# Optimization experiments

Measured on AMD Instinct MI355X. Metric: run time of the kernel, lower is better.

Reference implementation:

```python
import jax, jax.numpy as jnp
import numpy as np

N = 65536      # nodes
E = 1048576    # edges (avg degree 16)
L = 24         # input_length == lstm input size == lstm num_layers
H = 64         # lstm hidden


def _lin_init(key, fi, fo):
    return jax.random.normal(key, (fi, fo), jnp.float32) / np.sqrt(fi)


def setup_inputs() -> dict:
    key = jax.random.key(0)
    ks = iter(jax.random.split(key, 64))
    d = {}
    d["x"] = jax.random.normal(next(ks), (N, 421 + L), jnp.float32)
    d["edge_index"] = jax.random.randint(next(ks), (2, E), 0, N)

    def lin(fi, fo):
        return _lin_init(next(ks), fi, fo), jnp.zeros((fo,), jnp.float32)

    d["poi1_W"], d["poi1_b"] = lin(13, 64)
    d["poi2_W"], d["poi2_b"] = lin(64, 64)
    d["svi1_W"], d["svi1_b"] = lin(365, 128)
    d["svi2_W"], d["svi2_b"] = lin(128, 128)
    d["all1_W"], d["all1_b"] = lin(192, 128)
    d["all2_W"], d["all2_b"] = lin(128, 128)
    for name, fi, fo in (("gat1", 128, 128), ("gat2", 128, 128), ("gat3", 128, 64)):
        d[name + "_W"], d[name + "_b"] = lin(fi, fo)
        d[name + "_asrc"] = jax.random.normal(next(ks), (fo,), jnp.float32) / np.sqrt(fo)
        d[name + "_adst"] = jax.random.normal(next(ks), (fo,), jnp.float32) / np.sqrt(fo)
    d["lstm_Wih0"] = jax.random.normal(next(ks), (L, 4 * H), jnp.float32) / np.sqrt(L)
    d["lstm_Wih"] = jax.random.normal(next(ks), (L - 1, H, 4 * H), jnp.float32) / np.sqrt(H)
    d["lstm_Whh"] = jax.random.normal(next(ks), (L, H, 4 * H), jnp.float32) / np.sqrt(H)
    d["lstm_b"] = jnp.zeros((L, 4 * H), jnp.float32)
    d["time1_W"], d["time1_b"] = lin(64, 64)
    d["time2_W"], d["time2_b"] = lin(64, 64)
    d["lin1_W"], d["lin1_b"] = lin(128, 64)
    d["lin2_W"], d["lin2_b"] = lin(64, 64)
    d["lin3_W"], d["lin3_b"] = lin(64, 1)
    return d


def _gat(h_in, W, a_src, a_dst, b, src, dst, n):
    # PyG GATConv (1 head): gather -> per-edge attn -> segment softmax -> scatter
    h = h_in @ W                                   # [N, F]
    s = h @ a_src                                  # [N]
    t = h @ a_dst                                  # [N]
    e = jax.nn.leaky_relu(s[src] + t[dst], 0.2)    # [E']
    m = jax.ops.segment_max(e, dst, num_segments=n)
    ee = jnp.exp(e - m[dst])
    denom = jax.ops.segment_sum(ee, dst, num_segments=n)
    alpha = ee / denom[dst]
    out = jax.ops.segment_sum(h[src] * alpha[:, None], dst, num_segments=n)
    return out + b


def _forward(x, poi1_W, poi1_b, poi2_W, poi2_b, svi1_W, svi1_b, svi2_W, svi2_b,
             all1_W, all1_b, all2_W, all2_b,
             gat1_W, gat1_b, gat1_asrc, gat1_adst,
             gat2_W, gat2_b, gat2_asrc, gat2_adst,
             gat3_W, gat3_b, gat3_asrc, gat3_adst,
             lstm_Wih0, lstm_Wih, lstm_Whh, lstm_b,
             time1_W, time1_b, time2_W, time2_b,
             lin1_W, lin1_b, lin2_W, lin2_b, lin3_W, lin3_b,
             edge_index):
    n = x.shape[0]
    relu = jax.nn.relu
    # feature-branch MLPs
    x_poi = relu(relu(x[:, 3:16] @ poi1_W + poi1_b) @ poi2_W + poi2_b)
    x_svi = relu(relu(x[:, 56:421] @ svi1_W + svi1_b) @ svi2_W + svi2_b)
    h = jnp.concatenate([x_poi, x_svi], axis=1)
    h = relu(relu(h @ all1_W + all1_b) @ all2_W + all2_b)
    # add self loops once (PyG GATConv default add_self_loops=True)
    loops = jnp.arange(n, dtype=edge_index.dtype)
    src = jnp.concatenate([edge_index[0], loops])
    dst = jnp.concatenate([edge_index[1], loops])
    h = relu(_gat(h, gat1_W, gat1_asrc, gat1_adst, gat1_b, src, dst, n))
    h = relu(_gat(h, gat2_W, gat2_asrc, gat2_adst, gat2_b, src, dst, n))
    h = relu(_gat(h, gat3_W, gat3_asrc, gat3_adst, gat3_b, src, dst, n))
    # stacked LSTM over the single timestep t (h0=c0=0 -> f gate & Whh contribute 0)
    inp = x[:, 421:]                               # [N, L]
    hs = []
    for l in range(L):
        Wih = lstm_Wih0 if l == 0 else lstm_Wih[l - 1]
        gates = inp @ Wih + lstm_b[l]              # [N, 4H], torch gate order i,f,g,o
        i, f, g, o = jnp.split(gates, 4, axis=-1)
        c = jax.nn.sigmoid(i) * jnp.tanh(g)
        h_l = jax.nn.sigmoid(o) * jnp.tanh(c)
        hs.append(h_l)
        inp = h_l
    t = hs[2]                                      # hn[2]
    t = relu(relu(t @ time1_W + time1_b) @ time2_W + time2_b)
    z = jnp.concatenate([h, t], axis=1)            # [N, 128]
    z = relu(z @ lin1_W + lin1_b)
    z = relu(z @ lin2_W + lin2_b)
    return z @ lin3_W + lin3_b                     # [N, 1]


def reference(x, edge_index, poi1_W, poi1_b, poi2_W, poi2_b, svi1_W, svi1_b,
              svi2_W, svi2_b, all1_W, all1_b, all2_W, all2_b,
              gat1_W, gat1_b, gat1_asrc, gat1_adst,
              gat2_W, gat2_b, gat2_asrc, gat2_adst,
              gat3_W, gat3_b, gat3_asrc, gat3_adst,
              lstm_Wih0, lstm_Wih, lstm_Whh, lstm_b,
              time1_W, time1_b, time2_W, time2_b,
              lin1_W, lin1_b, lin2_W, lin2_b, lin3_W, lin3_b):
    return _forward(x, poi1_W, poi1_b, poi2_W, poi2_b, svi1_W, svi1_b, svi2_W, svi2_b,
                    all1_W, all1_b, all2_W, all2_b,
                    gat1_W, gat1_b, gat1_asrc, gat1_adst,
                    gat2_W, gat2_b, gat2_asrc, gat2_adst,
                    gat3_W, gat3_b, gat3_asrc, gat3_adst,
                    lstm_Wih0, lstm_Wih, lstm_Whh, lstm_b,
                    time1_W, time1_b, time2_W, time2_b,
                    lin1_W, lin1_b, lin2_W, lin2_b, lin3_W, lin3_b,
                    edge_index)
```

## Files before the change

kernel.cpp:

```cpp
#include <hip/hip_runtime.h>
#include <math.h>

#define DEV __device__ __forceinline__

typedef __attribute__((ext_vector_type(8))) short short8;
typedef __attribute__((ext_vector_type(4))) float f32x4;
typedef float f32x4u __attribute__((ext_vector_type(4), aligned(4)));
typedef __attribute__((ext_vector_type(4))) unsigned int u32x4;
typedef __attribute__((ext_vector_type(4))) _Float16 h16x4;

#define NEG_BIG (-3.0e38f)
#define CAPB 4096
#define CHUNK 4096

DEV float sigm(float x) { return 1.0f / (1.0f + __expf(-x)); }
DEV float leaky(float e) { return (e >= 0.0f) ? e : 0.2f * e; }

DEV void split_bf16(const float f[8], short8& hi, short8& lo) {
#pragma unroll
  for (int i = 0; i < 8; ++i) {
    unsigned u = __builtin_bit_cast(unsigned, f[i]);
    hi[i] = (short)(u >> 16);
    float h = __builtin_bit_cast(float, u & 0xffff0000u);
    float r = f[i] - h;
    lo[i] = (short)(__builtin_bit_cast(unsigned, r) >> 16);
  }
}

DEV unsigned packsplit(float v) {
  unsigned u = __builtin_bit_cast(unsigned, v);
  unsigned hf = u & 0xffff0000u;
  float r = v - __builtin_bit_cast(float, hf);
  return hf | (__builtin_bit_cast(unsigned, r) >> 16);
}

DEV void unpack_pk(const u32x4 p0, const u32x4 p1, short8& hi, short8& lo) {
  u32x4 h, l;
  h[0] = __builtin_amdgcn_perm(p0[1], p0[0], 0x07060302u);
  h[1] = __builtin_amdgcn_perm(p0[3], p0[2], 0x07060302u);
  h[2] = __builtin_amdgcn_perm(p1[1], p1[0], 0x07060302u);
  h[3] = __builtin_amdgcn_perm(p1[3], p1[2], 0x07060302u);
  l[0] = __builtin_amdgcn_perm(p0[1], p0[0], 0x05040100u);
  l[1] = __builtin_amdgcn_perm(p0[3], p0[2], 0x05040100u);
  l[2] = __builtin_amdgcn_perm(p1[1], p1[0], 0x05040100u);
  l[3] = __builtin_amdgcn_perm(p1[3], p1[2], 0x05040100u);
  hi = __builtin_bit_cast(short8, h);
  lo = __builtin_bit_cast(short8, l);
}

template <int G, int MT, int NT>
DEV void mfma_grp(f32x4 (&acc)[MT][NT], const short8 (&ah)[MT],
                  const short8 (&al)[MT], const short8 (&bh)[4],
                  const short8 (&bl)[4]) {
#pragma unroll
  for (int mt = 0; mt < MT; ++mt)
#pragma unroll
    for (int j = 0; j < 4; ++j) {
      acc[mt][G * 4 + j] = __builtin_amdgcn_mfma_f32_16x16x32_bf16(
          ah[mt], bh[j], acc[mt][G * 4 + j], 0, 0, 0);
      acc[mt][G * 4 + j] = __builtin_amdgcn_mfma_f32_16x16x32_bf16(
          ah[mt], bl[j], acc[mt][G * 4 + j], 0, 0, 0);
      acc[mt][G * 4 + j] = __builtin_amdgcn_mfma_f32_16x16x32_bf16(
          al[mt], bh[j], acc[mt][G * 4 + j], 0, 0, 0);
    }
}


__global__ void fill_i32_kernel(int* p, int v, int n) {
  int i = blockIdx.x * blockDim.x + threadIdx.x;
  if (i < n) p[i] = v;
}


__global__ __launch_bounds__(256) void bucket_bin(
    const int* __restrict__ ei, int* __restrict__ bucket_cnt,
    unsigned* __restrict__ ebuf, int E, int Et) {
  __shared__ unsigned stage[CHUNK];
  __shared__ int hist[512], rbase[512], lcur[512];
  const int tid = threadIdx.x;
  const long long e0 = (long long)blockIdx.x * CHUNK;
  const int nalive = (int)((Et - e0) < CHUNK ? (Et - e0) : CHUNK);
  for (int i = tid; i < 512; i += 256) hist[i] = 0;
  __syncthreads();
  for (int k = tid; k < nalive; k += 256) {
    long long e = e0 + k;
    int s, d;
    if (e < E) { s = ei[e]; d = ei[E + e]; } else { s = (int)(e - E); d = s; }
    unsigned p = (unsigned)s | ((unsigned)d << 16);
    stage[k] = p;
    atomicAdd(&hist[d >> 7], 1);
  }
  __syncthreads();
  for (int i = tid; i < 512; i += 256) {
    int c = hist[i];
    rbase[i] = c ? atomicAdd(&bucket_cnt[i], c) : 0;
    lcur[i] = 0;
  }
  __syncthreads();
  for (int k = tid; k < nalive; k += 256) {
    unsigned p = stage[k];
    int b = (int)(p >> 23);
    int lofs = atomicAdd(&lcur[b], 1);
    int pos = rbase[b] + lofs;
    if (pos < CAPB) ebuf[(long long)b * CAPB + pos] = p;
  }
}

__global__ __launch_bounds__(512) void bucket_scan(
    const int* __restrict__ cnt, int* __restrict__ start, int Et) {
  __shared__ int sh[512];
  int tid = threadIdx.x;
  int v = cnt[tid];
  sh[tid] = v;
  __syncthreads();
  int val = v;
  for (int off = 1; off < 512; off <<= 1) {
    int add = (tid >= off) ? sh[tid - off] : 0;
    __syncthreads();
    val += add;
    sh[tid] = val;
    __syncthreads();
  }
  start[tid] = val - v;
  if (tid == 511) start[512] = Et;
}

__global__ __launch_bounds__(128) void bucket_csr(
    const unsigned* __restrict__ ebuf, const int* __restrict__ bucket_cnt,
    const int* __restrict__ bucket_start, int* __restrict__ row_start,
    int* __restrict__ srcs, int N, int Et) {
  __shared__ unsigned stage[CAPB];
  __shared__ int hist[128], hbase[128], lcur[128];
  const int b = blockIdx.x, tid = threadIdx.x;
  int cnt = bucket_cnt[b];
  cnt = cnt < CAPB ? cnt : CAPB;
  const int gbase = bucket_start[b];
  hist[tid] = 0;
  __syncthreads();
  const unsigned* eb = ebuf + (long long)b * CAPB;
  for (int k = tid; k < cnt; k += 128) {
    unsigned p = eb[k];
    stage[k] = p;
    atomicAdd(&hist[(p >> 16) & 127], 1);
  }
  __syncthreads();
  int v = hist[tid];
  hbase[tid] = v;
  __syncthreads();
  int val = v;
  for (int off = 1; off < 128; off <<= 1) {
    int add = (tid >= off) ? hbase[tid - off] : 0;
    __syncthreads();
    val += add;
    hbase[tid] = val;
    __syncthreads();
  }
  int ex = val - v;
  row_start[b * 128 + tid] = gbase + ex;
  __syncthreads();
  hbase[tid] = ex;
  lcur[tid] = 0;
  __syncthreads();
  for (int k = tid; k < cnt; k += 128) {
    unsigned p = stage[k];
    int o = (p >> 16) & 127;
    int lofs = atomicAdd(&lcur[o], 1);
    srcs[gbase + hbase[o] + lofs] = (int)(p & 0xffffu);
  }
  if (b == 0 && tid == 0) row_start[N] = Et;
}

struct WJobs {
  const float* W[16];
  short* hi[16];
  short* lo[16];
  int K[16];
  int M16[16];
  int ldw[16];
  int skip[16];
  int tile0[16];
};

__global__ __launch_bounds__(64) void wsplit_all(WJobs jb, int njobs) {
  int b = blockIdx.x;
  int ji = 0;
#pragma unroll
  for (int i = 1; i < 16; ++i)
    if (i < njobs && b >= jb.tile0[i]) ji = i;
  int t = b - jb.tile0[ji];
  int M16 = jb.M16[ji];
  int kc = t / M16, ntG = t % M16;
  int K = jb.K[ji], ldw = jb.ldw[ji];
  const float* __restrict__ W = jb.W[ji];

  int lane = threadIdx.x;
  int kb = kc * 32 + (lane >> 4) * 8;
  int c = ntG * 16 + (lane & 15);
  if (jb.skip[ji] && c >= 64) c += 64;
  float f[8];
#pragma unroll
  for (int j = 0; j < 8; ++j) {
    int k = kb + j;
    f[j] = (k < K) ? W[(long long)k * ldw + c] : 0.0f;
  }
  short8 h, l;
  split_bf16(f, h, l);
  long long off = ((long long)t * 64 + lane) * 8;
  *(short8*)(jb.hi[ji] + off) = h;
  *(short8*)(jb.lo[ji] + off) = l;
}

template <int MT, int NT, int APK, int OPK, int STE>
__global__ __launch_bounds__(64) void gemm_mfma(
    const void* __restrict__ Av, int lda,
    const short* __restrict__ wh, const short* __restrict__ wl,
    const float* __restrict__ bias,
    void* __restrict__ Cv, int ldc,
    int K, int KC, int act,
    const float* __restrict__ asrc, const float* __restrict__ adst,
    float* __restrict__ sOut, float* __restrict__ tOut) {
  const int lane = threadIdx.x;
  const int m = lane & 15, q = lane >> 4;
  const long long r0 = (long long)blockIdx.x * (MT * 16);

  f32x4 acc[MT][NT];
#pragma unroll
  for (int i = 0; i < MT; ++i)
#pragma unroll
    for (int j = 0; j < NT; ++j) acc[i][j] = (f32x4)(0.0f);

  u32x4 pA[MT][2];
  float fA[MT][8];

  auto loadA = [&](int kc) {
#pragma unroll
    for (int mt = 0; mt < MT; ++mt) {
      if (APK == 1) {
        const unsigned* ap =
            (const unsigned*)Av + (r0 + mt * 16 + m) * lda + kc * 32 + q * 8;
        pA[mt][0] = *(const u32x4*)ap;
        pA[mt][1] = *(const u32x4*)(ap + 4);
      } else {
        const float* ap =
            (const float*)Av + (r0 + mt * 16 + m) * lda + kc * 32 + q * 8;
        if (kc * 32 + 32 <= K) {
          f32x4u p0 = *(const f32x4u*)ap;
          f32x4u p1 = *(const f32x4u*)(ap + 4);
#pragma unroll
          for (int j = 0; j < 4; ++j) { fA[mt][j] = p0[j]; fA[mt][4 + j] = p1[j]; }
        } else {
#pragma unroll
          for (int j = 0; j < 8; ++j) {
            int k = kc * 32 + q * 8 + j;
            fA[mt][j] = (k < K) ? ap[j] : 0.0f;
          }
        }
      }
    }
  };

  short8 ah[MT], al[MT];
  auto unpackA = [&]() {
#pragma unroll
    for (int mt = 0; mt < MT; ++mt) {
      if (APK == 1)
        unpack_pk(pA[mt][0], pA[mt][1], ah[mt], al[mt]);
      else
        split_bf16(fA[mt], ah[mt], al[mt]);
    }
  };

  short8 bh0[4], bl0[4], bh1[4], bl1[4];
  auto loadB = [&](short8 (&bh)[4], short8 (&bl)[4], int kc, int g) {
#pragma unroll
    for (int j = 0; j < 4; ++j) {
      long long off = (((long long)kc * NT + (g * 4 + j)) * 64 + lane) * 8;
      bh[j] = *(const short8*)(wh + off);
      bl[j] = *(const short8*)(wl + off);
    }
  };

  if constexpr (NT == 4) {
    loadA(0);
    loadB(bh0, bl0, 0, 0);
    int kc = 0;
    for (; kc + 2 <= KC; kc += 2) {
      unpackA();
      loadB(bh1, bl1, kc + 1, 0);
      loadA(kc + 1);
      mfma_grp<0, MT, NT>(acc, ah, al, bh0, bl0);
      unpackA();
      if (kc + 2 < KC) {
        loadB(bh0, bl0, kc + 2, 0);
        loadA(kc + 2);
      }
      mfma_grp<0, MT, NT>(acc, ah, al, bh1, bl1);
    }
    if (kc < KC) {
      unpackA();
      mfma_grp<0, MT, NT>(acc, ah, al, bh0, bl0);
    }
  } else {
    loadA(0);
    loadB(bh0, bl0, 0, 0);
    for (int kc = 0; kc < KC; ++kc) {
      unpackA();
      loadB(bh1, bl1, kc, 1);
      if (kc + 1 < KC) loadA(kc + 1);
      mfma_grp<0, MT, NT>(acc, ah, al, bh0, bl0);
      if (kc + 1 < KC) loadB(bh0, bl0, kc + 1, 0);
      mfma_grp<1, MT, NT>(acc, ah, al, bh1, bl1);
    }
  }

  if (STE == 2) {
    float w3[NT], bs[NT];
#pragma unroll
    for (int nt = 0; nt < NT; ++nt) {
      int col = nt * 16 + m;
      w3[nt] = asrc[col];
      bs[nt] = bias[col];
    }
#pragma unroll
    for (int mt = 0; mt < MT; ++mt)
#pragma unroll
      for (int reg = 0; reg < 4; ++reg) {
        float ps = 0.0f;
#pragma unroll
        for (int nt = 0; nt < NT; ++nt) {
          float v = fmaxf(acc[mt][nt][reg] + bs[nt], 0.0f);
          ps = fmaf(v, w3[nt], ps);
        }
#pragma unroll
        for (int off = 1; off < 16; off <<= 1) ps += __shfl_xor(ps, off, 64);
        if (m == 0) sOut[r0 + mt * 16 + q * 4 + reg] = ps + adst[0];
      }
    return;
  }

#pragma unroll
  for (int nt = 0; nt < NT; ++nt) {
    int col = nt * 16 + m;
    float bsv = bias ? bias[col] : 0.0f;
#pragma unroll
    for (int mt = 0; mt < MT; ++mt) {
      long long rb = r0 + mt * 16 + q * 4;
#pragma unroll
      for (int reg = 0; reg < 4; ++reg) {
        float v = acc[mt][nt][reg] + bsv;
        if (act == 1) v = fmaxf(v, 0.0f);
        if (OPK == 1)
          ((unsigned*)Cv)[(rb + reg) * ldc + col] = packsplit(v);
        else if (OPK == 2)
          ((_Float16*)Cv)[(rb + reg) * ldc + col] = (_Float16)v;
        else
          ((float*)Cv)[(rb + reg) * ldc + col] = v;
      }
    }
  }

  if (STE == 1) {
    float as[NT], ad[NT];
#pragma unroll
    for (int nt = 0; nt < NT; ++nt) {
      int col = nt * 16 + m;
      as[nt] = asrc[col];
      ad[nt] = adst[col];
    }
#pragma unroll
    for (int mt = 0; mt < MT; ++mt)
#pragma unroll
      for (int reg = 0; reg < 4; ++reg) {
        float ps = 0.0f, pt = 0.0f;
#pragma unroll
        for (int nt = 0; nt < NT; ++nt) {
          ps = fmaf(acc[mt][nt][reg], as[nt], ps);
          pt = fmaf(acc[mt][nt][reg], ad[nt], pt);
        }
#pragma unroll
        for (int off = 1; off < 16; off <<= 1) {
          ps += __shfl_xor(ps, off, 64);
          pt += __shfl_xor(pt, off, 64);
        }
        if (m == 0) {
          long long r = r0 + mt * 16 + q * 4 + reg;
          sOut[r] = ps;
          tOut[r] = pt;
        }
      }
  }
}

template <int APK>
__global__ __launch_bounds__(64) void gemm_lstm(
    const void* __restrict__ Av, int lda,
    const short* __restrict__ wh, const short* __restrict__ wl,
    const float* __restrict__ bias,
    unsigned* __restrict__ H,
    int K, int KC) {
  const int lane = threadIdx.x;
  const int m = lane & 15, q = lane >> 4;
  const long long r0 = (long long)blockIdx.x * 16;

  f32x4 acc[12];
#pragma unroll
  for (int j = 0; j < 12; ++j) acc[j] = (f32x4)(0.0f);

  u32x4 pA[2];
  float fA[8];

  auto loadA = [&](int kc) {
    if (APK == 1) {
      const unsigned* ap = (const unsigned*)Av + (r0 + m) * lda + kc * 32 + q * 8;
      pA[0] = *(const u32x4*)ap;
      pA[1] = *(const u32x4*)(ap + 4);
    } else {
      const float* ap = (const float*)Av + (r0 + m) * lda + kc * 32 + q * 8;
      if (kc * 32 + 32 <= K) {
        f32x4u p0 = *(const f32x4u*)ap;
        f32x4u p1 = *(const f32x4u*)(ap + 4);
#pragma unroll
        for (int j = 0; j < 4; ++j) { fA[j] = p0[j]; fA[4 + j] = p1[j]; }
      } else {
#pragma unroll
        for (int j = 0; j < 8; ++j) {
          int k = kc * 32 + q * 8 + j;
          fA[j] = (k < K) ? ap[j] : 0.0f;
        }
      }
    }
  };

  short8 bh0, bl0, bh1, bl1;
  auto loadB = [&](short8& bh, short8& bl, int kc, int nt) {
    long long off = (((long long)kc * 12 + nt) * 64 + lane) * 8;
    bh = *(const short8*)(wh + off);
    bl = *(const short8*)(wl + off);
  };

  loadA(0);
  loadB(bh0, bl0, 0, 0);
  for (int kc = 0; kc < KC; ++kc) {
    short8 ah, al;
    if (APK == 1)
      unpack_pk(pA[0], pA[1], ah, al);
    else
      split_bf16(fA, ah, al);
    loadB(bh1, bl1, kc, 1);
    if (kc + 1 < KC) loadA(kc + 1);
    const int kn = (kc + 1 < KC) ? kc + 1 : kc;
#pragma unroll
    for (int nt = 0; nt < 12; ++nt) {
      short8& cbh = (nt & 1) ? bh1 : bh0;
      short8& cbl = (nt & 1) ? bl1 : bl0;
      acc[nt] = __builtin_amdgcn_mfma_f32_16x16x32_bf16(ah, cbh, acc[nt], 0, 0, 0);
      acc[nt] = __builtin_amdgcn_mfma_f32_16x16x32_bf16(ah, cbl, acc[nt], 0, 0, 0);
      acc[nt] = __builtin_amdgcn_mfma_f32_16x16x32_bf16(al, cbh, acc[nt], 0, 0, 0);
      if (nt + 2 < 12)
        loadB((nt & 1) ? bh1 : bh0, (nt & 1) ? bl1 : bl0, kc, nt + 2);
      else if (nt + 2 == 12)
        loadB(bh0, bl0, kn, 0);
    }
  }

#pragma unroll
  for (int nt = 0; nt < 4; ++nt) {
    int col = nt * 16 + m;
    float bi = bias[col], bg = bias[128 + col], bo = bias[192 + col];
#pragma unroll
    for (int reg = 0; reg < 4; ++reg) {
      float gi = acc[nt][reg] + bi;
      float gg = acc[nt + 4][reg] + bg;
      float go = acc[nt + 8][reg] + bo;
      float cc = sigm(gi) * tanhf(gg);
      H[(r0 + q * 4 + reg) * 64 + col] = packsplit(sigm(go) * tanhf(cc));
    }
  }
}


template <int FO, int OPK>
__global__ __launch_bounds__(256) void gat_agg(
    const _Float16* __restrict__ G, const float* __restrict__ s,
    const float* __restrict__ t, const int* __restrict__ row_start,
    const int* __restrict__ srcs, const float* __restrict__ bias,
    void* __restrict__ outv, int ldc) {
  constexpr int CAP = 128;
  constexpr int LPE = FO / 4;
  constexpr int EPW = 64 / LPE;
  __shared__ float ecache[4][CAP];
  __shared__ int icache[4][CAP];
  const int wv = threadIdx.x >> 6;
  const int lane = threadIdx.x & 63;
  const int d = blockIdx.x * 4 + wv;
  const int start = row_start[d], end = row_start[d + 1];
  const float td = t[d];

  float m = NEG_BIG, dsum = 0.0f;
  for (int j = start + lane; j < end; j += 64) {
    int sj = srcs[j];
    float e = leaky(s[sj] + td);
    int idx = j - start;
    if (idx < CAP) { ecache[wv][idx] = e; icache[wv][idx] = sj; }
    float mn = fmaxf(m, e);
    dsum = dsum * __expf(m - mn) + __expf(e - mn);
    m = mn;
  }
#pragma unroll
  for (int off = 32; off; off >>= 1) {
    float mo = __shfl_xor(m, off, 64);
    float dso = __shfl_xor(dsum, off, 64);
    float mn = fmaxf(m, mo);
    dsum = dsum * __expf(m - mn) + dso * __expf(mo - mn);
    m = mn;
  }
  const float inv = 1.0f / dsum;

  const int deg = end - start;
  const int capdeg = deg < CAP ? deg : CAP;
  for (int idx = lane; idx < capdeg; idx += 64)
    ecache[wv][idx] = __expf(ecache[wv][idx] - m) * inv;
  __syncthreads();

  const int grp = lane / LPE, cl = lane % LPE;
  const _Float16* __restrict__ Gc = G + cl * 4;
  float a0 = 0.0f, a1 = 0.0f, a2 = 0.0f, a3 = 0.0f;
  int idx = grp;
  for (; idx + 3 * EPW < capdeg; idx += 4 * EPW) {
    const int i1 = idx + EPW, i2 = idx + 2 * EPW, i3 = idx + 3 * EPW;
    int s0 = icache[wv][idx], s1 = icache[wv][i1];
    int s2 = icache[wv][i2], s3 = icache[wv][i3];
    float l0 = ecache[wv][idx], l1 = ecache[wv][i1];
    float l2 = ecache[wv][i2], l3 = ecache[wv][i3];
    h16x4 g0 = *(const h16x4*)(Gc + (long long)s0 * FO);
    h16x4 g1 = *(const h16x4*)(Gc + (long long)s1 * FO);
    h16x4 g2 = *(const h16x4*)(Gc + (long long)s2 * FO);
    h16x4 g3 = *(const h16x4*)(Gc + (long long)s3 * FO);
    a0 = fmaf(l0, (float)g0[0], a0); a1 = fmaf(l0, (float)g0[1], a1);
    a2 = fmaf(l0, (float)g0[2], a2); a3 = fmaf(l0, (float)g0[3], a3);
    a0 = fmaf(l1, (float)g1[0], a0); a1 = fmaf(l1, (float)g1[1], a1);
    a2 = fmaf(l1, (float)g1[2], a2); a3 = fmaf(l1, (float)g1[3], a3);
    a0 = fmaf(l2, (float)g2[0], a0); a1 = fmaf(l2, (float)g2[1], a1);
    a2 = fmaf(l2, (float)g2[2], a2); a3 = fmaf(l2, (float)g2[3], a3);
    a0 = fmaf(l3, (float)g3[0], a0); a1 = fmaf(l3, (float)g3[1], a1);
    a2 = fmaf(l3, (float)g3[2], a2); a3 = fmaf(l3, (float)g3[3], a3);
  }
  for (; idx + EPW < capdeg; idx += 2 * EPW) {
    const int i1 = idx + EPW;
    int s0 = icache[wv][idx], s1 = icache[wv][i1];
    float l0 = ecache[wv][idx], l1 = ecache[wv][i1];
    h16x4 g0 = *(const h16x4*)(Gc + (long long)s0 * FO);
    h16x4 g1 = *(const h16x4*)(Gc + (long long)s1 * FO);
    a0 = fmaf(l0, (float)g0[0], a0); a1 = fmaf(l0, (float)g0[1], a1);
    a2 = fmaf(l0, (float)g0[2], a2); a3 = fmaf(l0, (float)g0[3], a3);
    a0 = fmaf(l1, (float)g1[0], a0); a1 = fmaf(l1, (float)g1[1], a1);
    a2 = fmaf(l1, (float)g1[2], a2); a3 = fmaf(l1, (float)g1[3], a3);
  }
  for (; idx < capdeg; idx += EPW) {
    int s0 = icache[wv][idx];
    float l0 = ecache[wv][idx];
    h16x4 g0 = *(const h16x4*)(Gc + (long long)s0 * FO);
    a0 = fmaf(l0, (float)g0[0], a0); a1 = fmaf(l0, (float)g0[1], a1);
    a2 = fmaf(l0, (float)g0[2], a2); a3 = fmaf(l0, (float)g0[3], a3);
  }
  for (; idx < deg; idx += EPW) {
    int s0 = srcs[start + idx];
    float l0 = __expf(leaky(s[s0] + td) - m) * inv;
    h16x4 g0 = *(const h16x4*)(Gc + (long long)s0 * FO);
    a0 = fmaf(l0, (float)g0[0], a0); a1 = fmaf(l0, (float)g0[1], a1);
    a2 = fmaf(l0, (float)g0[2], a2); a3 = fmaf(l0, (float)g0[3], a3);
  }
#pragma unroll
  for (int off = 32; off >= LPE; off >>= 1) {
    a0 += __shfl_xor(a0, off, 64);
    a1 += __shfl_xor(a1, off, 64);
    a2 += __shfl_xor(a2, off, 64);
    a3 += __shfl_xor(a3, off, 64);
  }
  if (grp == 0) {
    f32x4u bs = *(const f32x4u*)(bias + cl * 4);
    float v0 = fmaxf(a0 + bs[0], 0.0f);
    float v1 = fmaxf(a1 + bs[1], 0.0f);
    float v2 = fmaxf(a2 + bs[2], 0.0f);
    float v3 = fmaxf(a3 + bs[3], 0.0f);
    if (OPK == 1) {
      u32x4 pv;
      pv[0] = packsplit(v0); pv[1] = packsplit(v1);
      pv[2] = packsplit(v2); pv[3] = packsplit(v3);
      *(u32x4*)((unsigned*)outv + (long long)d * ldc + cl * 4) = pv;
    } else {
      f32x4u v; v[0] = v0; v[1] = v1; v[2] = v2; v[3] = v3;
      *(f32x4u*)((float*)outv + (long long)d * ldc + cl * 4) = v;
    }
  }
}


struct WSplit { const short* hi; const short* lo; };

extern "C" void kernel_launch(void* const* d_in, const int* in_sizes, int n_in,
                              void* d_out, int out_size, void* d_ws, size_t ws_size,
                              hipStream_t stream) {
  const int N = 65536, E = 1048576;
  const int Et = E + N;

  const float* x        = (const float*)d_in[0];
  const int*   ei       = (const int*)d_in[1];
  const float* poi1_W   = (const float*)d_in[2];
  const float* poi1_b   = (const float*)d_in[3];
  const float* poi2_W   = (const float*)d_in[4];
  const float* poi2_b   = (const float*)d_in[5];
  const float* svi1_W   = (const float*)d_in[6];
  const float* svi1_b   = (const float*)d_in[7];
  const float* svi2_W   = (const float*)d_in[8];
  const float* svi2_b   = (const float*)d_in[9];
  const float* all1_W   = (const float*)d_in[10];
  const float* all1_b   = (const float*)d_in[11];
  const float* all2_W   = (const float*)d_in[12];
  const float* all2_b   = (const float*)d_in[13];
  const float* gat1_W   = (const float*)d_in[14];
  const float* gat1_b   = (const float*)d_in[15];
  const float* gat1_as  = (const float*)d_in[16];
  const float* gat1_ad  = (const float*)d_in[17];
  const float* gat2_W   = (const float*)d_in[18];
  const float* gat2_b   = (const float*)d_in[19];
  const float* gat2_as  = (const float*)d_in[20];
  const float* gat2_ad  = (const float*)d_in[21];
  const float* gat3_W   = (const float*)d_in[22];
  const float* gat3_b   = (const float*)d_in[23];
  const float* gat3_as  = (const float*)d_in[24];
  const float* gat3_ad  = (const float*)d_in[25];
  const float* lstm_Wih0= (const float*)d_in[26];
  const float* lstm_Wih = (const float*)d_in[27];
  const float* lstm_b   = (const float*)d_in[29];
  const float* time1_W  = (const float*)d_in[30];
  const float* time1_b  = (const float*)d_in[31];
  const float* time2_W  = (const float*)d_in[32];
  const float* time2_b  = (const float*)d_in[33];
  const float* lin1_W   = (const float*)d_in[34];
  const float* lin1_b   = (const float*)d_in[35];
  const float* lin2_W   = (const float*)d_in[36];
  const float* lin2_b   = (const float*)d_in[37];
  const float* lin3_W   = (const float*)d_in[38];
  const float* lin3_b   = (const float*)d_in[39];
  float* out = (float*)d_out;

  float* wsf   = (float*)d_ws;
  float* R192  = wsf;
  float* RA    = R192 + (size_t)N * 192;
  float* RA2   = RA + (size_t)N * 64;
  float* RB    = RA + (size_t)N * 128;
  float* Rz    = RB + (size_t)N * 256;
  float* sArr  = Rz + (size_t)N * 128;
  float* tArr  = sArr + N;
  int* ints         = (int*)(tArr + N);
  int* row_start    = ints;
  int* srcs         = row_start + (N + 1);
  int* bucket_cnt   = srcs + Et;
  int* bucket_start = bucket_cnt + 512;
  unsigned* ebuf    = (unsigned*)(bucket_start + 513);
  short* pool = (short*)(((uintptr_t)(ebuf + 512 * CAPB) + 15) & ~(uintptr_t)15);

  WJobs jb{};
  int nj = 0, tiles = 0;
  auto split = [&](const float* W, int K, int M, int ldw, int skip) -> WSplit {
    int KC = (K + 31) / 32;
    size_t sz = (size_t)KC * M * 32;
    short* hi = pool; pool += sz;
    short* lo = pool; pool += sz;
    jb.W[nj] = W; jb.hi[nj] = hi; jb.lo[nj] = lo;
    jb.K[nj] = K; jb.M16[nj] = M / 16; jb.ldw[nj] = ldw; jb.skip[nj] = skip;
    jb.tile0[nj] = tiles;
    tiles += KC * (M / 16);
    ++nj;
    return {hi, lo};
  };

  auto gemm = [&](const void* A, int lda, WSplit w, const float* bias,
                  void* C, int ldc, int K, int M, int act, int apk, int opk) {
    int KC = (K + 31) / 32;
    dim3 grid(N / 16), blk(64);
    if (M == 64) {
      if (apk == 0 && opk == 1)
        hipLaunchKernelGGL((gemm_mfma<1, 4, 0, 1, 0>), grid, blk, 0, stream,
                           A, lda, w.hi, w.lo, bias, C, ldc, K, KC, act,
                           nullptr, nullptr, nullptr, nullptr);
      else if (apk == 1 && opk == 1)
        hipLaunchKernelGGL((gemm_mfma<1, 4, 1, 1, 0>), grid, blk, 0, stream,
                           A, lda, w.hi, w.lo, bias, C, ldc, K, KC, act,
                           nullptr, nullptr, nullptr, nullptr);
      else if (apk == 1 && opk == 0)
        hipLaunchKernelGGL((gemm_mfma<1, 4, 1, 0, 0>), grid, blk, 0, stream,
                           A, lda, w.hi, w.lo, bias, C, ldc, K, KC, act,
                           nullptr, nullptr, nullptr, nullptr);
      else
        hipLaunchKernelGGL((gemm_mfma<1, 4, 0, 0, 0>), grid, blk, 0, stream,
                           A, lda, w.hi, w.lo, bias, C, ldc, K, KC, act,
                           nullptr, nullptr, nullptr, nullptr);
    } else {
      if (apk == 0 && opk == 1)
        hipLaunchKernelGGL((gemm_mfma<1, 8, 0, 1, 0>), grid, blk, 0, stream,
                           A, lda, w.hi, w.lo, bias, C, ldc, K, KC, act,
                           nullptr, nullptr, nullptr, nullptr);
      else if (apk == 1 && opk == 1)
        hipLaunchKernelGGL((gemm_mfma<1, 8, 1, 1, 0>), grid, blk, 0, stream,
                           A, lda, w.hi, w.lo, bias, C, ldc, K, KC, act,
                           nullptr, nullptr, nullptr, nullptr);
      else if (apk == 1 && opk == 0)
        hipLaunchKernelGGL((gemm_mfma<1, 8, 1, 0, 0>), grid, blk, 0, stream,
                           A, lda, w.hi, w.lo, bias, C, ldc, K, KC, act,
                           nullptr, nullptr, nullptr, nullptr);
      else
        hipLaunchKernelGGL((gemm_mfma<1, 8, 0, 0, 0>), grid, blk, 0, stream,
                           A, lda, w.hi, w.lo, bias, C, ldc, K, KC, act,
                           nullptr, nullptr, nullptr, nullptr);
    }
  };
  auto gemm_st = [&](const void* A, WSplit w, void* G, int M,
                     const float* as_, const float* ad_) {
    dim3 grid(N / 16), blk(64);
    if (M == 128)
      hipLaunchKernelGGL((gemm_mfma<1, 8, 1, 2, 1>), grid, blk, 0, stream,
                         A, 128, w.hi, w.lo, (const float*)nullptr,
                         G, 128, 128, 4, 0, as_, ad_, sArr, tArr);
    else
      hipLaunchKernelGGL((gemm_mfma<1, 4, 1, 2, 1>), grid, blk, 0, stream,
                         A, 128, w.hi, w.lo, (const float*)nullptr,
                         G, 64, 128, 4, 0, as_, ad_, sArr, tArr);
  };

  WSplit wpoi1 = split(poi1_W, 13, 64, 64, 0);
  WSplit wpoi2 = split(poi2_W, 64, 64, 64, 0);
  WSplit wsvi1 = split(svi1_W, 365, 128, 128, 0);
  WSplit wsvi2 = split(svi2_W, 128, 128, 128, 0);
  WSplit wall1 = split(all1_W, 192, 128, 128, 0);
  WSplit wall2 = split(all2_W, 128, 128, 128, 0);
  WSplit wg1   = split(gat1_W, 128, 128, 128, 0);
  WSplit wg2   = split(gat2_W, 128, 128, 128, 0);
  WSplit wg3   = split(gat3_W, 128, 64, 64, 0);
  WSplit wls0  = split(lstm_Wih0, 24, 192, 256, 1);
  WSplit wls1  = split(lstm_Wih, 64, 192, 256, 1);
  WSplit wls2  = split(lstm_Wih + 64 * 256, 64, 192, 256, 1);
  WSplit wt1   = split(time1_W, 64, 64, 64, 0);
  WSplit wt2   = split(time2_W, 64, 64, 64, 0);
  WSplit wl1   = split(lin1_W, 128, 64, 64, 0);
  WSplit wl2   = split(lin2_W, 64, 64, 64, 0);
  hipLaunchKernelGGL(wsplit_all, dim3(tiles), dim3(64), 0, stream, jb, nj);

  const int TB = 256;

  hipLaunchKernelGGL(fill_i32_kernel, dim3(2), dim3(TB), 0, stream,
                     bucket_cnt, 0, 512);
  hipLaunchKernelGGL(bucket_bin, dim3((Et + CHUNK - 1) / CHUNK), dim3(256),
                     0, stream, ei, bucket_cnt, ebuf, E, Et);
  hipLaunchKernelGGL(bucket_scan, dim3(1), dim3(512), 0, stream,
                     bucket_cnt, bucket_start, Et);
  hipLaunchKernelGGL(bucket_csr, dim3(512), dim3(128), 0, stream,
                     ebuf, bucket_cnt, bucket_start, row_start, srcs, N, Et);

  gemm(x + 3, 445, wpoi1, poi1_b, RA, 64, 13, 64, 1, 0, 1);
  gemm(RA, 64, wpoi2, poi2_b, R192, 192, 64, 64, 1, 1, 1);
  gemm(x + 56, 445, wsvi1, svi1_b, RB, 128, 365, 128, 1, 0, 1);
  gemm(RB, 128, wsvi2, svi2_b, R192 + 64, 192, 128, 128, 1, 1, 1);
  gemm(R192, 192, wall1, all1_b, RA, 128, 192, 128, 1, 1, 1);
  gemm(RA, 128, wall2, all2_b, RB, 128, 128, 128, 1, 1, 1);

  const int aggBlocks = N / 4;
  _Float16* Gh = (_Float16*)RA;

  gemm_st(RB, wg1, Gh, 128, gat1_as, gat1_ad);
  hipLaunchKernelGGL((gat_agg<128, 1>), dim3(aggBlocks), dim3(256), 0, stream,
                     Gh, sArr, tArr, row_start, srcs, gat1_b, RB, 128);
  gemm_st(RB, wg2, Gh, 128, gat2_as, gat2_ad);
  hipLaunchKernelGGL((gat_agg<128, 1>), dim3(aggBlocks), dim3(256), 0, stream,
                     Gh, sArr, tArr, row_start, srcs, gat2_b, RB, 128);
  gemm_st(RB, wg3, Gh, 64, gat3_as, gat3_ad);
  hipLaunchKernelGGL((gat_agg<64, 1>), dim3(aggBlocks), dim3(256), 0, stream,
                     Gh, sArr, tArr, row_start, srcs, gat3_b, Rz, 128);

  hipLaunchKernelGGL((gemm_lstm<0>), dim3(N / 16), dim3(64), 0, stream,
                     x + 421, 445, wls0.hi, wls0.lo, lstm_b,
                     (unsigned*)RA, 24, 1);
  hipLaunchKernelGGL((gemm_lstm<1>), dim3(N / 16), dim3(64), 0, stream,
                     RA, 64, wls1.hi, wls1.lo, lstm_b + 256,
                     (unsigned*)RA2, 64, 2);
  hipLaunchKernelGGL((gemm_lstm<1>), dim3(N / 16), dim3(64), 0, stream,
                     RA2, 64, wls2.hi, wls2.lo, lstm_b + 512,
                     (unsigned*)RA, 64, 2);

  gemm(RA, 64, wt1, time1_b, RA2, 64, 64, 64, 1, 1, 1);
  gemm(RA2, 64, wt2, time2_b, Rz + 64, 128, 64, 64, 1, 1, 1);

  gemm(Rz, 128, wl1, lin1_b, RA, 64, 128, 64, 1, 1, 1);
  hipLaunchKernelGGL((gemm_mfma<1, 4, 1, 0, 2>), dim3(N / 16), dim3(64), 0, stream,
                     RA, 64, wl2.hi, wl2.lo, lin2_b, nullptr, 64, 64, 2, 0,
                     lin3_W, lin3_b, out, nullptr);
}
```

Baseline: 686.2 us.

## Co-schedule independent GEMM and LSTM branches in combined multi-role kernel launches

```diff
diff --git a/kernel.cpp b/kernel.cpp
--- a/kernel.cpp
+++ b/kernel.cpp
@@ -210,18 +210,24 @@
   *(short8*)(jb.lo[ji] + off) = l;
 }
 
+
+struct GemmArgs {
+  const void* A; const short* wh; const short* wl; const float* bias;
+  void* C; const float* asrc; const float* adst; float* sOut; float* tOut;
+  int lda, ldc, K, KC, act;
+};
+
+struct LstmArgs {
+  const void* A; const short* wh; const short* wl; const float* bias;
+  unsigned* H; int lda, K, KC;
+};
+
 template <int MT, int NT, int APK, int OPK, int STE>
-__global__ __launch_bounds__(64) void gemm_mfma(
-    const void* __restrict__ Av, int lda,
-    const short* __restrict__ wh, const short* __restrict__ wl,
-    const float* __restrict__ bias,
-    void* __restrict__ Cv, int ldc,
-    int K, int KC, int act,
-    const float* __restrict__ asrc, const float* __restrict__ adst,
-    float* __restrict__ sOut, float* __restrict__ tOut) {
+DEV void gemm_body(const GemmArgs& g, int bid) {
   const int lane = threadIdx.x;
   const int m = lane & 15, q = lane >> 4;
-  const long long r0 = (long long)blockIdx.x * (MT * 16);
+  const long long r0 = (long long)bid * (MT * 16);
+  const int K = g.K, KC = g.KC, lda = g.lda;
 
   f32x4 acc[MT][NT];
 #pragma unroll
@@ -237,12 +243,12 @@
     for (int mt = 0; mt < MT; ++mt) {
       if (APK == 1) {
         const unsigned* ap =
-            (const unsigned*)Av + (r0 + mt * 16 + m) * lda + kc * 32 + q * 8;
+            (const unsigned*)g.A + (r0 + mt * 16 + m) * lda + kc * 32 + q * 8;
         pA[mt][0] = *(const u32x4*)ap;
         pA[mt][1] = *(const u32x4*)(ap + 4);
       } else {
         const float* ap =
-            (const float*)Av + (r0 + mt * 16 + m) * lda + kc * 32 + q * 8;
+            (const float*)g.A + (r0 + mt * 16 + m) * lda + kc * 32 + q * 8;
         if (kc * 32 + 32 <= K) {
           f32x4u p0 = *(const f32x4u*)ap;
           f32x4u p1 = *(const f32x4u*)(ap + 4);
@@ -271,12 +277,12 @@
   };
 
   short8 bh0[4], bl0[4], bh1[4], bl1[4];
-  auto loadB = [&](short8 (&bh)[4], short8 (&bl)[4], int kc, int g) {
+  auto loadB = [&](short8 (&bh)[4], short8 (&bl)[4], int kc, int gg) {
 #pragma unroll
     for (int j = 0; j < 4; ++j) {
-      long long off = (((long long)kc * NT + (g * 4 + j)) * 64 + lane) * 8;
-      bh[j] = *(const short8*)(wh + off);
-      bl[j] = *(const short8*)(wl + off);
+      long long off = (((long long)kc * NT + (gg * 4 + j)) * 64 + lane) * 8;
+      bh[j] = *(const short8*)(g.wh + off);
+      bl[j] = *(const short8*)(g.wl + off);
     }
   };
 
@@ -318,8 +324,8 @@
 #pragma unroll
     for (int nt = 0; nt < NT; ++nt) {
       int col = nt * 16 + m;
-      w3[nt] = asrc[col];
-      bs[nt] = bias[col];
+      w3[nt] = g.asrc[col];
+      bs[nt] = g.bias[col];
     }
 #pragma unroll
     for (int mt = 0; mt < MT; ++mt)
@@ -333,7 +339,7 @@
         }
 #pragma unroll
         for (int off = 1; off < 16; off <<= 1) ps += __shfl_xor(ps, off, 64);
-        if (m == 0) sOut[r0 + mt * 16 + q * 4 + reg] = ps + adst[0];
+        if (m == 0) g.sOut[r0 + mt * 16 + q * 4 + reg] = ps + g.adst[0];
       }
     return;
   }
@@ -341,20 +347,20 @@
 #pragma unroll
   for (int nt = 0; nt < NT; ++nt) {
     int col = nt * 16 + m;
-    float bsv = bias ? bias[col] : 0.0f;
+    float bsv = g.bias ? g.bias[col] : 0.0f;
 #pragma unroll
     for (int mt = 0; mt < MT; ++mt) {
       long long rb = r0 + mt * 16 + q * 4;
 #pragma unroll
       for (int reg = 0; reg < 4; ++reg) {
         float v = acc[mt][nt][reg] + bsv;
-        if (act == 1) v = fmaxf(v, 0.0f);
+        if (g.act == 1) v = fmaxf(v, 0.0f);
         if (OPK == 1)
-          ((unsigned*)Cv)[(rb + reg) * ldc + col] = packsplit(v);
+          ((unsigned*)g.C)[(rb + reg) * g.ldc + col] = packsplit(v);
         else if (OPK == 2)
-          ((_Float16*)Cv)[(rb + reg) * ldc + col] = (_Float16)v;
+          ((_Float16*)g.C)[(rb + reg) * g.ldc + col] = (_Float16)v;
         else
-          ((float*)Cv)[(rb + reg) * ldc + col] = v;
+          ((float*)g.C)[(rb + reg) * g.ldc + col] = v;
       }
     }
   }
@@ -364,8 +370,8 @@
 #pragma unroll
     for (int nt = 0; nt < NT; ++nt) {
       int col = nt * 16 + m;
-      as[nt] = asrc[col];
-      ad[nt] = adst[col];
+      as[nt] = g.asrc[col];
+      ad[nt] = g.adst[col];
     }
 #pragma unroll
     for (int mt = 0; mt < MT; ++mt)
@@ -384,23 +390,19 @@
         }
         if (m == 0) {
           long long r = r0 + mt * 16 + q * 4 + reg;
-          sOut[r] = ps;
-          tOut[r] = pt;
+          g.sOut[r] = ps;
+          g.tOut[r] = pt;
         }
       }
   }
 }
 
 template <int APK>
-__global__ __launch_bounds__(64) void gemm_lstm(
-    const void* __restrict__ Av, int lda,
-    const short* __restrict__ wh, const short* __restrict__ wl,
-    const float* __restrict__ bias,
-    unsigned* __restrict__ H,
-    int K, int KC) {
+DEV void lstm_body(const LstmArgs& g, int bid) {
   const int lane = threadIdx.x;
   const int m = lane & 15, q = lane >> 4;
-  const long long r0 = (long long)blockIdx.x * 16;
+  const long long r0 = (long long)bid * 16;
+  const int K = g.K, KC = g.KC, lda = g.lda;
 
   f32x4 acc[12];
 #pragma unroll
@@ -411,11 +413,11 @@
 
   auto loadA = [&](int kc) {
     if (APK == 1) {
-      const unsigned* ap = (const unsigned*)Av + (r0 + m) * lda + kc * 32 + q * 8;
+      const unsigned* ap = (const unsigned*)g.A + (r0 + m) * lda + kc * 32 + q * 8;
       pA[0] = *(const u32x4*)ap;
       pA[1] = *(const u32x4*)(ap + 4);
     } else {
-      const float* ap = (const float*)Av + (r0 + m) * lda + kc * 32 + q * 8;
+      const float* ap = (const float*)g.A + (r0 + m) * lda + kc * 32 + q * 8;
       if (kc * 32 + 32 <= K) {
         f32x4u p0 = *(const f32x4u*)ap;
         f32x4u p1 = *(const f32x4u*)(ap + 4);
@@ -434,8 +436,8 @@
   short8 bh0, bl0, bh1, bl1;
   auto loadB = [&](short8& bh, short8& bl, int kc, int nt) {
     long long off = (((long long)kc * 12 + nt) * 64 + lane) * 8;
-    bh = *(const short8*)(wh + off);
-    bl = *(const short8*)(wl + off);
+    bh = *(const short8*)(g.wh + off);
+    bl = *(const short8*)(g.wl + off);
   };
 
   loadA(0);
@@ -466,16 +468,54 @@
 #pragma unroll
   for (int nt = 0; nt < 4; ++nt) {
     int col = nt * 16 + m;
-    float bi = bias[col], bg = bias[128 + col], bo = bias[192 + col];
+    float bi = g.bias[col], bg = g.bias[128 + col], bo = g.bias[192 + col];
 #pragma unroll
     for (int reg = 0; reg < 4; ++reg) {
       float gi = acc[nt][reg] + bi;
       float gg = acc[nt + 4][reg] + bg;
       float go = acc[nt + 8][reg] + bo;
       float cc = sigm(gi) * tanhf(gg);
-      H[(r0 + q * 4 + reg) * 64 + col] = packsplit(sigm(go) * tanhf(cc));
-    }
-  }
+      g.H[(r0 + q * 4 + reg) * 64 + col] = packsplit(sigm(go) * tanhf(cc));
+    }
+  }
+}
+
+
+template <int MT, int NT, int APK, int OPK, int STE>
+__global__ __launch_bounds__(64) void gemm_mfma(GemmArgs g) {
+  gemm_body<MT, NT, APK, OPK, STE>(g, blockIdx.x);
+}
+
+template <int NTa, int APKa, int OPKa, int STEa,
+          int NTb, int APKb, int OPKb, int STEb>
+__global__ __launch_bounds__(64) void combo_gg(GemmArgs a, GemmArgs b, int nA) {
+  int bid = blockIdx.x;
+  if (bid < nA)
+    gemm_body<2, NTa, APKa, OPKa, STEa>(a, bid);
+  else
+    gemm_body<2, NTb, APKb, OPKb, STEb>(b, bid - nA);
+}
+
+template <int NTa, int APKa, int OPKa, int STEa, int LAPK>
+__global__ __launch_bounds__(64) void combo_gl(GemmArgs a, LstmArgs l, int nA) {
+  int bid = blockIdx.x;
+  if (bid < nA)
+    gemm_body<2, NTa, APKa, OPKa, STEa>(a, bid);
+  else
+    lstm_body<LAPK>(l, bid - nA);
+}
+
+template <int NTa, int APKa, int OPKa, int STEa,
+          int NTb, int APKb, int OPKb, int STEb, int LAPK>
+__global__ __launch_bounds__(64) void combo_ggl(GemmArgs a, GemmArgs b,
+                                                LstmArgs l, int nA, int nAB) {
+  int bid = blockIdx.x;
+  if (bid < nA)
+    gemm_body<2, NTa, APKa, OPKa, STEa>(a, bid);
+  else if (bid < nAB)
+    gemm_body<2, NTb, APKb, OPKb, STEb>(b, bid - nA);
+  else
+    lstm_body<LAPK>(l, bid - nAB);
 }
 
 
@@ -648,10 +688,11 @@
   float* wsf   = (float*)d_ws;
   float* R192  = wsf;
   float* RA    = R192 + (size_t)N * 192;
-  float* RA2   = RA + (size_t)N * 64;
   float* RB    = RA + (size_t)N * 128;
-  float* Rz    = RB + (size_t)N * 256;
-  float* sArr  = Rz + (size_t)N * 128;
+  float* Rz    = RB + (size_t)N * 128;
+  float* LA    = Rz + (size_t)N * 128;
+  float* LB    = LA + (size_t)N * 64;
+  float* sArr  = LB + (size_t)N * 64;
   float* tArr  = sArr + N;
   int* ints         = (int*)(tArr + N);
   int* row_start    = ints;
@@ -676,57 +717,22 @@
     return {hi, lo};
   };
 
-  auto gemm = [&](const void* A, int lda, WSplit w, const float* bias,
-                  void* C, int ldc, int K, int M, int act, int apk, int opk) {
-    int KC = (K + 31) / 32;
-    dim3 grid(N / 16), blk(64);
-    if (M == 64) {
-      if (apk == 0 && opk == 1)
-        hipLaunchKernelGGL((gemm_mfma<1, 4, 0, 1, 0>), grid, blk, 0, stream,
-                           A, lda, w.hi, w.lo, bias, C, ldc, K, KC, act,
-                           nullptr, nullptr, nullptr, nullptr);
-      else if (apk == 1 && opk == 1)
-        hipLaunchKernelGGL((gemm_mfma<1, 4, 1, 1, 0>), grid, blk, 0, stream,
-                           A, lda, w.hi, w.lo, bias, C, ldc, K, KC, act,
-                           nullptr, nullptr, nullptr, nullptr);
-      else if (apk == 1 && opk == 0)
-        hipLaunchKernelGGL((gemm_mfma<1, 4, 1, 0, 0>), grid, blk, 0, stream,
-                           A, lda, w.hi, w.lo, bias, C, ldc, K, KC, act,
-                           nullptr, nullptr, nullptr, nullptr);
-      else
-        hipLaunchKernelGGL((gemm_mfma<1, 4, 0, 0, 0>), grid, blk, 0, stream,
-                           A, lda, w.hi, w.lo, bias, C, ldc, K, KC, act,
-                           nullptr, nullptr, nullptr, nullptr);
-    } else {
-      if (apk == 0 && opk == 1)
-        hipLaunchKernelGGL((gemm_mfma<1, 8, 0, 1, 0>), grid, blk, 0, stream,
-                           A, lda, w.hi, w.lo, bias, C, ldc, K, KC, act,
-                           nullptr, nullptr, nullptr, nullptr);
-      else if (apk == 1 && opk == 1)
-        hipLaunchKernelGGL((gemm_mfma<1, 8, 1, 1, 0>), grid, blk, 0, stream,
-                           A, lda, w.hi, w.lo, bias, C, ldc, K, KC, act,
-                           nullptr, nullptr, nullptr, nullptr);
-      else if (apk == 1 && opk == 0)
-        hipLaunchKernelGGL((gemm_mfma<1, 8, 1, 0, 0>), grid, blk, 0, stream,
-                           A, lda, w.hi, w.lo, bias, C, ldc, K, KC, act,
-                           nullptr, nullptr, nullptr, nullptr);
-      else
-        hipLaunchKernelGGL((gemm_mfma<1, 8, 0, 0, 0>), grid, blk, 0, stream,
-                           A, lda, w.hi, w.lo, bias, C, ldc, K, KC, act,
-                           nullptr, nullptr, nullptr, nullptr);
-    }
+  auto mkg = [&](const void* A, int lda, WSplit w, const float* bias, void* C,
+                 int ldc, int K, int act, const float* as_ = nullptr,
+                 const float* ad_ = nullptr, float* sO = nullptr,
+                 float* tO = nullptr) -> GemmArgs {
+    GemmArgs g;
+    g.A = A; g.lda = lda; g.wh = w.hi; g.wl = w.lo; g.bias = bias;
+    g.C = C; g.ldc = ldc; g.K = K; g.KC = (K + 31) / 32; g.act = act;
+    g.asrc = as_; g.adst = ad_; g.sOut = sO; g.tOut = tO;
+    return g;
   };
-  auto gemm_st = [&](const void* A, WSplit w, void* G, int M,
-                     const float* as_, const float* ad_) {
-    dim3 grid(N / 16), blk(64);
-    if (M == 128)
-      hipLaunchKernelGGL((gemm_mfma<1, 8, 1, 2, 1>), grid, blk, 0, stream,
-                         A, 128, w.hi, w.lo, (const float*)nullptr,
-                         G, 128, 128, 4, 0, as_, ad_, sArr, tArr);
-    else
-      hipLaunchKernelGGL((gemm_mfma<1, 4, 1, 2, 1>), grid, blk, 0, stream,
-                         A, 128, w.hi, w.lo, (const float*)nullptr,
-                         G, 64, 128, 4, 0, as_, ad_, sArr, tArr);
+  auto mkl = [&](const void* A, int lda, WSplit w, const float* bias,
+                 unsigned* H, int K) -> LstmArgs {
+    LstmArgs l;
+    l.A = A; l.lda = lda; l.wh = w.hi; l.wl = w.lo; l.bias = bias;
+    l.H = H; l.K = K; l.KC = (K + 31) / 32;
+    return l;
   };
 
   WSplit wpoi1 = split(poi1_W, 13, 64, 64, 0);
@@ -748,6 +754,8 @@
   hipLaunchKernelGGL(wsplit_all, dim3(tiles), dim3(64), 0, stream, jb, nj);
 
   const int TB = 256;
+  const int GB = N / 32;
+  const int LBK = N / 16;
 
   hipLaunchKernelGGL(fill_i32_kernel, dim3(2), dim3(TB), 0, stream,
                      bucket_cnt, 0, 512);
@@ -758,41 +766,52 @@
   hipLaunchKernelGGL(bucket_csr, dim3(512), dim3(128), 0, stream,
                      ebuf, bucket_cnt, bucket_start, row_start, srcs, N, Et);
 
-  gemm(x + 3, 445, wpoi1, poi1_b, RA, 64, 13, 64, 1, 0, 1);
-  gemm(RA, 64, wpoi2, poi2_b, R192, 192, 64, 64, 1, 1, 1);
-  gemm(x + 56, 445, wsvi1, svi1_b, RB, 128, 365, 128, 1, 0, 1);
-  gemm(RB, 128, wsvi2, svi2_b, R192 + 64, 192, 128, 128, 1, 1, 1);
-  gemm(R192, 192, wall1, all1_b, RA, 128, 192, 128, 1, 1, 1);
-  gemm(RA, 128, wall2, all2_b, RB, 128, 128, 128, 1, 1, 1);
+  _Float16* Gh = (_Float16*)RA;
+
+  hipLaunchKernelGGL((combo_ggl<8, 0, 1, 0, 4, 0, 1, 0, 0>),
+                     dim3(GB + GB + LBK), dim3(64), 0, stream,
+                     mkg(x + 56, 445, wsvi1, svi1_b, RB, 128, 365, 1),
+                     mkg(x + 3, 445, wpoi1, poi1_b, RA, 64, 13, 1),
+                     mkl(x + 421, 445, wls0, lstm_b, (unsigned*)LA, 24),
+                     GB, GB + GB);
+  hipLaunchKernelGGL((combo_ggl<8, 1, 1, 0, 4, 1, 1, 0, 1>),
+                     dim3(GB + GB + LBK), dim3(64), 0, stream,
+                     mkg(RB, 128, wsvi2, svi2_b, R192 + 64, 192, 128, 1),
+                     mkg(RA, 64, wpoi2, poi2_b, R192, 192, 64, 1),
+                     mkl(LA, 64, wls1, lstm_b + 256, (unsigned*)LB, 64),
+                     GB, GB + GB);
+  hipLaunchKernelGGL((combo_gl<8, 1, 1, 0, 1>),
+                     dim3(GB + LBK), dim3(64), 0, stream,
+                     mkg(R192, 192, wall1, all1_b, RA, 128, 192, 1),
+                     mkl(LB, 64, wls2, lstm_b + 512, (unsigned*)LA, 64), GB);
+  hipLaunchKernelGGL((combo_gg<8, 1, 1, 0, 4, 1, 1, 0>),
+                     dim3(GB + GB), dim3(64), 0, stream,
+                     mkg(RA, 128, wall2, all2_b, RB, 128, 128, 1),
+                     mkg(LA, 64, wt1, time1_b, LB, 64, 64, 1), GB);
+  hipLaunchKernelGGL((combo_gg<8, 1, 2, 1, 4, 1, 1, 0>),
+                     dim3(GB + GB), dim3(64), 0, stream,
+                     mkg(RB, 128, wg1, nullptr, Gh, 128, 128, 0,
+                         gat1_as, gat1_ad, sArr, tArr),
+                     mkg(LB, 64, wt2, time2_b, Rz + 64, 128, 64, 1), GB);
 
   const int aggBlocks = N / 4;
-  _Float16* Gh = (_Float16*)RA;
-
-  gemm_st(RB, wg1, Gh, 128, gat1_as, gat1_ad);
+
   hipLaunchKernelGGL((gat_agg<128, 1>), dim3(aggBlocks), dim3(256), 0, stream,
                      Gh, sArr, tArr, row_start, srcs, gat1_b, RB, 128);
-  gemm_st(RB, wg2, Gh, 128, gat2_as, gat2_ad);
+  hipLaunchKernelGGL((gemm_mfma<2, 8, 1, 2, 1>), dim3(GB), dim3(64), 0, stream,
+                     mkg(RB, 128, wg2, nullptr, Gh, 128, 128, 0,
+                         gat2_as, gat2_ad, sArr, tArr));
   hipLaunchKernelGGL((gat_agg<128, 1>), dim3(aggBlocks), dim3(256), 0, stream,
                      Gh, sArr, tArr, row_start, srcs, gat2_b, RB, 128);
-  gemm_st(RB, wg3, Gh, 64, gat3_as, gat3_ad);
+  hipLaunchKernelGGL((gemm_mfma<2, 4, 1, 2, 1>), dim3(GB), dim3(64), 0, stream,
+                     mkg(RB, 128, wg3, nullptr, Gh, 64, 128, 0,
+                         gat3_as, gat3_ad, sArr, tArr));
   hipLaunchKernelGGL((gat_agg<64, 1>), dim3(aggBlocks), dim3(256), 0, stream,
                      Gh, sArr, tArr, row_start, srcs, gat3_b, Rz, 128);
 
-  hipLaunchKernelGGL((gemm_lstm<0>), dim3(N / 16), dim3(64), 0, stream,
-                     x + 421, 445, wls0.hi, wls0.lo, lstm_b,
-                     (unsigned*)RA, 24, 1);
-  hipLaunchKernelGGL((gemm_lstm<1>), dim3(N / 16), dim3(64), 0, stream,
-                     RA, 64, wls1.hi, wls1.lo, lstm_b + 256,
-                     (unsigned*)RA2, 64, 2);
-  hipLaunchKernelGGL((gemm_lstm<1>), dim3(N / 16), dim3(64), 0, stream,
-                     RA2, 64, wls2.hi, wls2.lo, lstm_b + 512,
-                     (unsigned*)RA, 64, 2);
-
-  gemm(RA, 64, wt1, time1_b, RA2, 64, 64, 64, 1, 1, 1);
-  gemm(RA2, 64, wt2, time2_b, Rz + 64, 128, 64, 64, 1, 1, 1);
-
-  gemm(Rz, 128, wl1, lin1_b, RA, 64, 128, 64, 1, 1, 1);
-  hipLaunchKernelGGL((gemm_mfma<1, 4, 1, 0, 2>), dim3(N / 16), dim3(64), 0, stream,
-                     RA, 64, wl2.hi, wl2.lo, lin2_b, nullptr, 64, 64, 2, 0,
-                     lin3_W, lin3_b, out, nullptr);
-}
+  hipLaunchKernelGGL((gemm_mfma<2, 4, 1, 1, 0>), dim3(GB), dim3(64), 0, stream,
+                     mkg(Rz, 128, wl1, lin1_b, RA, 64, 128, 1));
+  hipLaunchKernelGGL((gemm_mfma<2, 4, 1, 0, 2>), dim3(GB), dim3(64), 0, stream,
+                     mkg(RA, 64, wl2, lin2_b, nullptr, 64, 64, 2,
+                         lin3_W, lin3_b, out, nullptr));
+}
```

Result: faster. 648.5 us (-5.5%).
